# Kernel optimization log

Measured on AMD Instinct MI355X. Metric: run time of the kernel, lower is better.

The kernel has to match this reference:

```python
import jax, jax.numpy as jnp
import numpy as np

N = 50000  # nodes


def gcn_layer(x, src, dst, W, b):
    """DGL GraphConv with norm='both': D_in^{-1/2} A^T D_out^{-1/2} x W + b."""
    E = src.shape[0]
    ones = jnp.ones((E,), dtype=x.dtype)
    deg_out = jax.ops.segment_sum(ones, src, num_segments=N)  # out-degree of src nodes
    deg_in = jax.ops.segment_sum(ones, dst, num_segments=N)   # in-degree of dst nodes
    norm_src = jax.lax.rsqrt(jnp.maximum(deg_out, 1.0))
    norm_dst = jax.lax.rsqrt(jnp.maximum(deg_in, 1.0))
    h = x * norm_src[:, None]
    agg = jax.ops.segment_sum(h[src], dst, num_segments=N)  # [N, in_dim]
    return (agg @ W) * norm_dst[:, None] + b


def encoder(feat, src, dst, W1, b1, W2, b2):
    h = jax.nn.relu(gcn_layer(feat, src, dst, W1, b1))
    h = jax.nn.relu(gcn_layer(h, src, dst, W2, b2))
    return h


def proj(h, fc1_W, fc1_b, fc2_W, fc2_b):
    z = jax.nn.elu(h @ fc1_W + fc1_b)
    return z @ fc2_W + fc2_b


def setup_inputs() -> dict:
    key = jax.random.key(0)
    ks = jax.random.split(key, 12)
    in_dim, hid, out_dim, E = 128, 128, 128, 800000
    inp = {
        "feat1": jax.random.normal(ks[0], (N, in_dim), dtype=jnp.float32),
        "feat2": jax.random.normal(ks[1], (N, in_dim), dtype=jnp.float32),
        "edge_index1": jax.random.randint(ks[2], (2, E), 0, N),
        "edge_index2": jax.random.randint(ks[3], (2, E), 0, N),
        # GraphConv weights: in_dim -> 2*hid -> hid
        "conv1_W": jax.random.normal(ks[4], (in_dim, 2 * hid), dtype=jnp.float32) * 0.05,
        "conv1_b": jnp.zeros((2 * hid,), dtype=jnp.float32),
        "conv2_W": jax.random.normal(ks[5], (2 * hid, hid), dtype=jnp.float32) * 0.05,
        "conv2_b": jnp.zeros((hid,), dtype=jnp.float32),
        # MLP proj: fc1 hid->out, fc2 out->hid
        "fc1_W": jax.random.normal(ks[6], (hid, out_dim), dtype=jnp.float32) * 0.05,
        "fc1_b": jnp.zeros((out_dim,), dtype=jnp.float32),
        "fc2_W": jax.random.normal(ks[7], (out_dim, hid), dtype=jnp.float32) * 0.05,
        "fc2_b": jnp.zeros((hid,), dtype=jnp.float32),
    }
    return inp


def reference(feat1, feat2, edge_index1, edge_index2,
              conv1_W, conv1_b, conv2_W, conv2_b,
              fc1_W, fc1_b, fc2_W, fc2_b):
    h1 = encoder(feat1, edge_index1[0], edge_index1[1], conv1_W, conv1_b, conv2_W, conv2_b)
    h2 = encoder(feat2, edge_index2[0], edge_index2[1], conv1_W, conv1_b, conv2_W, conv2_b)
    z1 = proj(h1, fc1_W, fc1_b, fc2_W, fc2_b)
    z2 = proj(h2, fc1_W, fc1_b, fc2_W, fc2_b)
    return (z1, z2)
```

## Files before the change

### kernel.cpp

```cpp
#include <hip/hip_runtime.h>
#include <math.h>

#define NDIM 128
#define H2   256
#define MAXG 2
#define TPE  8192
#define NBKMAX 512

typedef __attribute__((ext_vector_type(8))) short bf16x8;
typedef __attribute__((ext_vector_type(4))) float f32x4;

__device__ __forceinline__ unsigned short f2bf(float f) {
    unsigned int u = __float_as_uint(f);
    u += 0x7fffu + ((u >> 16) & 1u);
    return (unsigned short)(u >> 16);
}
__device__ __forceinline__ float bf2f(unsigned short h) {
    return __uint_as_float(((unsigned int)h) << 16);
}
__device__ __forceinline__ void split2(float f, unsigned short& h, unsigned short& l) {
    h = f2bf(f);
    l = f2bf(f - bf2f(h));
}

struct BinArgs {
    const int* src[MAXG]; const int* dst[MAXG];
    int* histD[MAXG]; int* histS[MAXG];
    int* totD[MAXG];  int* baseD[MAXG];
    int* totS[MAXG];  int* baseS[MAXG];
    unsigned int* pairs[MAXG];
    unsigned short* srcS[MAXG];
    int E[MAXG]; int NBK; int NT; int n;
};

__global__ __launch_bounds__(256) void binA(BinArgs a) {
    __shared__ int cntD[NBKMAX], cntS[NBKMAX];
    int g = blockIdx.y, t = blockIdx.x, tid = threadIdx.x;
    for (int b = tid; b < NBKMAX; b += 256) { cntD[b] = 0; cntS[b] = 0; }
    __syncthreads();
    int E = a.E[g];
    int base = t * TPE;
#pragma unroll
    for (int k = 0; k < TPE / 256; ++k) {
        int e = base + k * 256 + tid;
        if (e < E) {
            atomicAdd(&cntD[a.dst[g][e] >> 7], 1);
            atomicAdd(&cntS[a.src[g][e] >> 7], 1);
        }
    }
    __syncthreads();
    for (int b = tid; b < a.NBK; b += 256) {
        a.histD[g][t * a.NBK + b] = cntD[b];
        a.histS[g][t * a.NBK + b] = cntS[b];
    }
}

__global__ __launch_bounds__(512) void binB(BinArgs a) {
    int g = blockIdx.y, side = blockIdx.z;
    int* hist = side ? a.histS[g] : a.histD[g];
    int* tot  = side ? a.totS[g]  : a.totD[g];
    int* base = side ? a.baseS[g] : a.baseD[g];
    __shared__ int s[512];
    int b = threadIdx.x;
    int v = 0;
    if (b < a.NBK)
        for (int t = 0; t < a.NT; ++t) v += hist[t * a.NBK + b];
    s[b] = v;
    __syncthreads();
    for (int off = 1; off < 512; off <<= 1) {
        int u = (b >= off) ? s[b - off] : 0;
        __syncthreads();
        s[b] += u;
        __syncthreads();
    }
    int excl = s[b] - v;
    if (b < a.NBK) {
        tot[b] = v;
        base[b] = excl;
        int run = excl;
        for (int t = 0; t < a.NT; ++t) {
            int h = hist[t * a.NBK + b];
            hist[t * a.NBK + b] = run;
            run += h;
        }
    }
}

__global__ __launch_bounds__(256) void binC(BinArgs a) {
    __shared__ int offD[NBKMAX], offS[NBKMAX];
    int g = blockIdx.y, t = blockIdx.x, tid = threadIdx.x;
    for (int b = tid; b < a.NBK; b += 256) {
        offD[b] = a.histD[g][t * a.NBK + b];
        offS[b] = a.histS[g][t * a.NBK + b];
    }
    __syncthreads();
    int E = a.E[g];
    int base = t * TPE;
    unsigned int* pairs = a.pairs[g];
    unsigned short* ss = a.srcS[g];
#pragma unroll
    for (int k = 0; k < TPE / 256; ++k) {
        int e = base + k * 256 + tid;
        if (e < E) {
            int s = a.src[g][e], d = a.dst[g][e];
            int pos = atomicAdd(&offD[d >> 7], 1);
            pairs[pos] = ((unsigned int)(d & 127) << 16) | (unsigned int)s;
            int posS = atomicAdd(&offS[s >> 7], 1);
            ss[posS] = (unsigned short)s;
        }
    }
}

struct FinArgs {
    const unsigned int* pairs[MAXG];
    const unsigned short* srcS[MAXG];
    const int* totD[MAXG]; const int* baseD[MAXG];
    const int* totS[MAXG]; const int* baseS[MAXG];
    int* row_ptr[MAXG]; int* row_end[MAXG];
    unsigned short* edge_srt[MAXG];
    float* ns[MAXG]; float* nd[MAXG];
    int n;
};

__global__ __launch_bounds__(256) void finalize(FinArgs a) {
    __shared__ int cnt[128], hist[128], scn[128], cur[128];
    int g = blockIdx.y, bkt = blockIdx.x, tid = threadIdx.x;
    if (tid < 128) { cnt[tid] = 0; hist[tid] = 0; }
    __syncthreads();
    {
        int base = a.baseS[g][bkt], tot = a.totS[g][bkt];
        const unsigned short* ss = a.srcS[g];
        for (int i = tid; i < tot; i += 256)
            atomicAdd(&cnt[ss[base + i] & 127], 1);
    }
    int cntE = a.totD[g][bkt], base = a.baseD[g][bkt];
    const unsigned int* pp = a.pairs[g] + base;
    for (int i = tid; i < cntE; i += 256)
        atomicAdd(&hist[pp[i] >> 16], 1);
    __syncthreads();
    if (tid < 128) {
        int node = bkt * 128 + tid;
        if (node < a.n) {
            int c = cnt[tid];
            a.ns[g][node] = rsqrtf((float)(c > 1 ? c : 1));
        }
        scn[tid] = hist[tid];
    }
    __syncthreads();
    for (int off = 1; off < 128; off <<= 1) {
        int v = (tid < 128 && tid >= off) ? scn[tid - off] : 0;
        __syncthreads();
        if (tid < 128) scn[tid] += v;
        __syncthreads();
    }
    if (tid < 128) {
        int incl = scn[tid];
        int h = hist[tid];
        cur[tid] = incl - h;
        int node = bkt * 128 + tid;
        if (node < a.n) {
            a.row_ptr[g][node] = base + incl - h;
            a.row_end[g][node] = base + incl;
            a.nd[g][node] = rsqrtf((float)(h > 1 ? h : 1));
        }
    }
    __syncthreads();
    for (int i = tid; i < cntE; i += 256) {
        unsigned int p = pp[i];
        int pos = atomicAdd(&cur[p >> 16], 1);
        a.edge_srt[g][base + pos] = (unsigned short)(p & 0xFFFF);
    }
}

struct GatherArgs {
    const float* X[MAXG];
    const int* row_ptr[MAXG]; const int* row_end[MAXG];
    const unsigned short* edge_src[MAXG];
    const float* nd[MAXG];
    const float* sns[MAXG];
    unsigned short* outH[MAXG]; unsigned short* outL[MAXG];
    const float* bias; int use_nd; int use_sns; int n;
};

__global__ __launch_bounds__(256) void gather_split_b(GatherArgs a) {
    int g = blockIdx.y;
    int half = threadIdx.x >> 5;
    int lane = threadIdx.x & 31;
    int r = blockIdx.x * 8 + half;
    if (r >= a.n) return;
    int j = a.row_ptr[g][r];
    int end = a.row_end[g][r];
    const unsigned short* ep = a.edge_src[g];
    const float* X = a.X[g];
    const float* sns = a.sns[g];
    int base = lane * 4;
    float4 acc = make_float4(0.f, 0.f, 0.f, 0.f);
    if (a.use_sns) {
        for (; j + 3 < end; j += 4) {
            int s0 = ep[j], s1 = ep[j + 1], s2 = ep[j + 2], s3 = ep[j + 3];
            float n0 = sns[s0], n1 = sns[s1], n2 = sns[s2], n3 = sns[s3];
            float4 v0 = *(const float4*)(X + (size_t)s0 * NDIM + base);
            float4 v1 = *(const float4*)(X + (size_t)s1 * NDIM + base);
            float4 v2 = *(const float4*)(X + (size_t)s2 * NDIM + base);
            float4 v3 = *(const float4*)(X + (size_t)s3 * NDIM + base);
            acc.x = fmaf(v0.x, n0, fmaf(v1.x, n1, fmaf(v2.x, n2, fmaf(v3.x, n3, acc.x))));
            acc.y = fmaf(v0.y, n0, fmaf(v1.y, n1, fmaf(v2.y, n2, fmaf(v3.y, n3, acc.y))));
            acc.z = fmaf(v0.z, n0, fmaf(v1.z, n1, fmaf(v2.z, n2, fmaf(v3.z, n3, acc.z))));
            acc.w = fmaf(v0.w, n0, fmaf(v1.w, n1, fmaf(v2.w, n2, fmaf(v3.w, n3, acc.w))));
        }
        for (; j < end; ++j) {
            int s0 = ep[j];
            float n0 = sns[s0];
            float4 v0 = *(const float4*)(X + (size_t)s0 * NDIM + base);
            acc.x = fmaf(v0.x, n0, acc.x); acc.y = fmaf(v0.y, n0, acc.y);
            acc.z = fmaf(v0.z, n0, acc.z); acc.w = fmaf(v0.w, n0, acc.w);
        }
    } else {
        for (; j + 3 < end; j += 4) {
            int s0 = ep[j], s1 = ep[j + 1], s2 = ep[j + 2], s3 = ep[j + 3];
            float4 v0 = *(const float4*)(X + (size_t)s0 * NDIM + base);
            float4 v1 = *(const float4*)(X + (size_t)s1 * NDIM + base);
            float4 v2 = *(const float4*)(X + (size_t)s2 * NDIM + base);
            float4 v3 = *(const float4*)(X + (size_t)s3 * NDIM + base);
            acc.x += v0.x + v1.x + v2.x + v3.x;
            acc.y += v0.y + v1.y + v2.y + v3.y;
            acc.z += v0.z + v1.z + v2.z + v3.z;
            acc.w += v0.w + v1.w + v2.w + v3.w;
        }
        for (; j < end; ++j) {
            int s0 = ep[j];
            float4 v0 = *(const float4*)(X + (size_t)s0 * NDIM + base);
            acc.x += v0.x; acc.y += v0.y; acc.z += v0.z; acc.w += v0.w;
        }
    }
    float v[4] = {acc.x, acc.y, acc.z, acc.w};
    if (a.use_nd) {
        float s = a.nd[g][r];
#pragma unroll
        for (int i = 0; i < 4; ++i)
            v[i] = fmaxf(v[i] * s + a.bias[base + i], 0.f);
    }
    unsigned short h[4], l[4];
#pragma unroll
    for (int i = 0; i < 4; ++i) split2(v[i], h[i], l[i]);
    *(ushort4*)(a.outH[g] + (size_t)r * NDIM + base) = make_ushort4(h[0], h[1], h[2], h[3]);
    *(ushort4*)(a.outL[g] + (size_t)r * NDIM + base) = make_ushort4(l[0], l[1], l[2], l[3]);
}

__global__ void wprep_all(const float* __restrict__ W1, const float* __restrict__ W2,
                          const float* __restrict__ F1, const float* __restrict__ F2,
                          unsigned short* __restrict__ W1h, unsigned short* __restrict__ W1l,
                          unsigned short* __restrict__ W2h, unsigned short* __restrict__ W2l,
                          unsigned short* __restrict__ F1h, unsigned short* __restrict__ F1l,
                          unsigned short* __restrict__ F2h, unsigned short* __restrict__ F2l) {
    int i = blockIdx.x * 256 + threadIdx.x;
    const float* Wsrc; unsigned short *Hd, *Ld; int K, Nc, idx;
    if (i < 32768)       { Wsrc = W1; Hd = W1h; Ld = W1l; K = 128; Nc = 256; idx = i; }
    else if (i < 65536)  { Wsrc = W2; Hd = W2h; Ld = W2l; K = 256; Nc = 128; idx = i - 32768; }
    else if (i < 81920)  { Wsrc = F1; Hd = F1h; Ld = F1l; K = 128; Nc = 128; idx = i - 65536; }
    else                 { Wsrc = F2; Hd = F2h; Ld = F2l; K = 128; Nc = 128; idx = i - 81920; }
    int k = idx / Nc, n = idx % Nc;
    unsigned short h, l;
    split2(Wsrc[idx], h, l);
    Hd[n * K + k] = h;
    Ld[n * K + k] = l;
}

struct GemmArgs {
    const unsigned short* Ah[MAXG]; const unsigned short* Al[MAXG];
    const unsigned short* Bh; const unsigned short* Bl;
    float* C[MAXG]; unsigned short* CH[MAXG]; unsigned short* CL[MAXG];
    const float* rsOut[MAXG]; const float* bOut;
    int M, K, Nc, act, has_rs, has_b, split_out;
};

template <int KT>
__global__ __launch_bounds__(256) void mfma_gemm_s(GemmArgs a) {
    constexpr int LDA = KT + 8;
    __shared__ __align__(16) unsigned short As_h[64 * LDA];
    __shared__ __align__(16) unsigned short As_l[64 * LDA];

    int g = blockIdx.z;
    const unsigned short* __restrict__ Ah_g = a.Ah[g];
    const unsigned short* __restrict__ Al_g = a.Al[g];
    const unsigned short* __restrict__ Bh = a.Bh;
    const unsigned short* __restrict__ Bl = a.Bl;

    int tid  = threadIdx.x;
    int wave = tid >> 6, lane = tid & 63;
    int quad = lane >> 4, l16 = lane & 15;
    int rowBase = blockIdx.x * 64;
    int colBase = blockIdx.y * 128;
    int M = a.M, Nc = a.Nc;

    f32x4 acc[4][2] = {};

    size_t boff[2];
#pragma unroll
    for (int j = 0; j < 2; ++j)
        boff[j] = (size_t)(colBase + wave * 32 + j * 16 + l16) * KT + quad * 8;

    bf16x8 bh[2][4], bl[2][4];
#pragma unroll
    for (int j = 0; j < 2; ++j)
#pragma unroll
        for (int kt = 0; kt < 4; ++kt) {
            bh[j][kt] = *(const bf16x8*)(Bh + boff[j] + kt * 32);
            bl[j][kt] = *(const bf16x8*)(Bl + boff[j] + kt * 32);
        }

    constexpr int CPR = KT / 8;
#pragma unroll
    for (int c0 = 0; c0 < 64 * CPR; c0 += 256) {
        int c = c0 + tid;
        int row = c / CPR;
        int col = (c - row * CPR) * 8;
        int gr = rowBase + row;
        uint4 vh = make_uint4(0, 0, 0, 0), vl = make_uint4(0, 0, 0, 0);
        if (gr < M) {
            vh = *(const uint4*)(Ah_g + (size_t)gr * KT + col);
            vl = *(const uint4*)(Al_g + (size_t)gr * KT + col);
        }
        *(uint4*)(As_h + row * LDA + col) = vh;
        *(uint4*)(As_l + row * LDA + col) = vl;
    }
    __syncthreads();

#pragma unroll
    for (int p = 0; p < KT / 128; ++p) {
        if (p) {
#pragma unroll
            for (int j = 0; j < 2; ++j)
#pragma unroll
                for (int kt = 0; kt < 4; ++kt) {
                    bh[j][kt] = *(const bf16x8*)(Bh + boff[j] + p * 128 + kt * 32);
                    bl[j][kt] = *(const bf16x8*)(Bl + boff[j] + p * 128 + kt * 32);
                }
        }
#pragma unroll
        for (int kt = 0; kt < 4; ++kt) {
            int kc = p * 128 + kt * 32 + quad * 8;
            bf16x8 af[4], alf[4];
#pragma unroll
            for (int i = 0; i < 4; ++i) {
                af[i]  = *(const bf16x8*)(As_h + (i * 16 + l16) * LDA + kc);
                alf[i] = *(const bf16x8*)(As_l + (i * 16 + l16) * LDA + kc);
            }
#pragma unroll
            for (int i = 0; i < 4; ++i)
#pragma unroll
                for (int j = 0; j < 2; ++j) {
                    acc[i][j] = __builtin_amdgcn_mfma_f32_16x16x32_bf16(af[i],  bh[j][kt], acc[i][j], 0, 0, 0);
                    acc[i][j] = __builtin_amdgcn_mfma_f32_16x16x32_bf16(alf[i], bh[j][kt], acc[i][j], 0, 0, 0);
                    acc[i][j] = __builtin_amdgcn_mfma_f32_16x16x32_bf16(af[i],  bl[j][kt], acc[i][j], 0, 0, 0);
                }
        }
    }

#pragma unroll
    for (int i = 0; i < 4; ++i) {
#pragma unroll
        for (int r = 0; r < 4; ++r) {
            int row = rowBase + i * 16 + quad * 4 + r;
            if (row >= M) continue;
            float rs = a.has_rs ? a.rsOut[g][row] : 1.0f;
#pragma unroll
            for (int j = 0; j < 2; ++j) {
                int col = colBase + wave * 32 + j * 16 + l16;
                float v = acc[i][j][r] * rs;
                if (a.has_b) v += a.bOut[col];
                if (a.act == 1) v = fmaxf(v, 0.f);
                else if (a.act == 2) v = v > 0.f ? v : expm1f(v);
                if (a.split_out) {
                    unsigned short h, l;
                    split2(v, h, l);
                    a.CH[g][(size_t)row * Nc + col] = h;
                    a.CL[g][(size_t)row * Nc + col] = l;
                } else {
                    a.C[g][(size_t)row * Nc + col] = v;
                }
            }
        }
    }
}

extern "C" void kernel_launch(void* const* d_in, const int* in_sizes, int n_in,
                              void* d_out, int out_size, void* d_ws, size_t ws_size,
                              hipStream_t stream) {
    const float* feat[2] = {(const float*)d_in[0], (const float*)d_in[1]};
    const int*   ei[2]   = {(const int*)d_in[2], (const int*)d_in[3]};
    const float* W1   = (const float*)d_in[4];
    const float* b1   = (const float*)d_in[5];
    const float* W2   = (const float*)d_in[6];
    const float* b2   = (const float*)d_in[7];
    const float* fc1W = (const float*)d_in[8];
    const float* fc1b = (const float*)d_in[9];
    const float* fc2W = (const float*)d_in[10];
    const float* fc2b = (const float*)d_in[11];
    int N = in_sizes[0] / NDIM;
    float* out = (float*)d_out;

    int Emax = 0;
    for (int g = 0; g < 2; ++g) { int E = in_sizes[2 + g] / 2; if (E > Emax) Emax = E; }
    int NBK = (N + 127) / 128;
    int NT  = (Emax + TPE - 1) / TPE;

    char* p = (char*)d_ws;
    float* ns_[2]; float* nd_[2];
    for (int i = 0; i < 2; ++i) { ns_[i] = (float*)p; p += (size_t)N * 4; }
    for (int i = 0; i < 2; ++i) { nd_[i] = (float*)p; p += (size_t)N * 4; }
    int* rp_[2]; int* re_[2]; unsigned short* esrt_[2];
    for (int i = 0; i < 2; ++i) { rp_[i] = (int*)p; p += (size_t)N * 4; }
    for (int i = 0; i < 2; ++i) { re_[i] = (int*)p; p += (size_t)N * 4; }
    for (int i = 0; i < 2; ++i) { esrt_[i] = (unsigned short*)p; p += (size_t)Emax * 2; }
    unsigned short* R1[2]; unsigned short* R2[2];
    for (int i = 0; i < 2; ++i) { R1[i] = (unsigned short*)p; p += (size_t)N * NDIM * 2 * 2; }
    for (int i = 0; i < 2; ++i) { R2[i] = (unsigned short*)p; p += (size_t)N * H2 * 2 * 2; }
    unsigned short* W1th = (unsigned short*)p; p += (size_t)NDIM * H2 * 2;
    unsigned short* W1tl = (unsigned short*)p; p += (size_t)NDIM * H2 * 2;
    unsigned short* W2th = (unsigned short*)p; p += (size_t)H2 * NDIM * 2;
    unsigned short* W2tl = (unsigned short*)p; p += (size_t)H2 * NDIM * 2;
    unsigned short* f1th = (unsigned short*)p; p += (size_t)NDIM * NDIM * 2;
    unsigned short* f1tl = (unsigned short*)p; p += (size_t)NDIM * NDIM * 2;
    unsigned short* f2th = (unsigned short*)p; p += (size_t)NDIM * NDIM * 2;
    unsigned short* f2tl = (unsigned short*)p; p += (size_t)NDIM * NDIM * 2;
    int* tb = (int*)p; p += (size_t)2 * 4 * NBK * 4;

    int* histD_[2]; int* histS_[2]; unsigned int* pairs_[2]; unsigned short* srcS_[2];
    for (int i = 0; i < 2; ++i) {
        histD_[i] = (int*)R2[i];
        histS_[i] = (int*)R2[i] + (size_t)NT * NBK;
        pairs_[i] = (unsigned int*)((char*)R2[i] + (1 << 20));
        srcS_[i]  = (unsigned short*)R1[i];
    }

    BinArgs ba = {};
    ba.NBK = NBK; ba.NT = NT; ba.n = N;
    for (int i = 0; i < 2; ++i) {
        int E = in_sizes[2 + i] / 2;
        ba.src[i] = ei[i]; ba.dst[i] = ei[i] + E; ba.E[i] = E;
        ba.histD[i] = histD_[i]; ba.histS[i] = histS_[i];
        ba.totD[i]  = tb + (size_t)i * 4 * NBK;
        ba.baseD[i] = tb + (size_t)i * 4 * NBK + NBK;
        ba.totS[i]  = tb + (size_t)i * 4 * NBK + 2 * NBK;
        ba.baseS[i] = tb + (size_t)i * 4 * NBK + 3 * NBK;
        ba.pairs[i] = pairs_[i]; ba.srcS[i] = srcS_[i];
    }

    wprep_all<<<384, 256, 0, stream>>>(W1, W2, fc1W, fc2W,
                                       W1th, W1tl, W2th, W2tl, f1th, f1tl, f2th, f2tl);
    binA<<<dim3(NT, 2), 256, 0, stream>>>(ba);
    binB<<<dim3(1, 2, 2), 512, 0, stream>>>(ba);
    binC<<<dim3(NT, 2), 256, 0, stream>>>(ba);

    FinArgs fa = {};
    fa.n = N;
    for (int i = 0; i < 2; ++i) {
        fa.pairs[i] = pairs_[i]; fa.srcS[i] = srcS_[i];
        fa.totD[i] = ba.totD[i]; fa.baseD[i] = ba.baseD[i];
        fa.totS[i] = ba.totS[i]; fa.baseS[i] = ba.baseS[i];
        fa.row_ptr[i] = rp_[i]; fa.row_end[i] = re_[i];
        fa.edge_srt[i] = esrt_[i];
        fa.ns[i] = ns_[i]; fa.nd[i] = nd_[i];
    }
    finalize<<<dim3(NBK, 2), 256, 0, stream>>>(fa);

    unsigned short *A1h[2], *A1l[2], *X1h[2], *X1l[2], *Gh[2], *Gl[2], *Zh[2], *Zl[2];
    float* T[2];
    for (int i = 0; i < 2; ++i) {
        A1h[i] = R1[i]; A1l[i] = R1[i] + (size_t)N * NDIM;
        T[i]   = (float*)R1[i];
        Zh[i]  = R1[i]; Zl[i]  = R1[i] + (size_t)N * NDIM;
        X1h[i] = R2[i]; X1l[i] = R2[i] + (size_t)N * H2;
        Gh[i]  = R2[i]; Gl[i]  = R2[i] + (size_t)N * NDIM;
    }

    int ggrid = (N + 7) / 8;
    int mgrid = (N + 63) / 64;

    GatherArgs ga = {};
    ga.n = N; ga.use_nd = 0; ga.use_sns = 1; ga.bias = b2;
    for (int i = 0; i < 2; ++i) {
        ga.X[i] = feat[i];
        ga.row_ptr[i] = rp_[i]; ga.row_end[i] = re_[i]; ga.edge_src[i] = esrt_[i];
        ga.nd[i] = nd_[i]; ga.sns[i] = ns_[i];
        ga.outH[i] = A1h[i]; ga.outL[i] = A1l[i];
    }
    gather_split_b<<<dim3(ggrid, 2), 256, 0, stream>>>(ga);

    GemmArgs g1 = {};
    g1.Bh = W1th; g1.Bl = W1tl; g1.bOut = b1;
    g1.M = N; g1.K = NDIM; g1.Nc = H2; g1.act = 1; g1.has_rs = 1; g1.has_b = 1; g1.split_out = 1;
    for (int i = 0; i < 2; ++i) {
        g1.Ah[i] = A1h[i]; g1.Al[i] = A1l[i];
        g1.CH[i] = X1h[i]; g1.CL[i] = X1l[i]; g1.rsOut[i] = nd_[i];
    }
    mfma_gemm_s<128><<<dim3(mgrid, H2 / 128, 2), 256, 0, stream>>>(g1);

    GemmArgs g2 = {};
    g2.Bh = W2th; g2.Bl = W2tl;
    g2.M = N; g2.K = H2; g2.Nc = NDIM; g2.act = 0; g2.has_rs = 1; g2.has_b = 0; g2.split_out = 0;
    for (int i = 0; i < 2; ++i) {
        g2.Ah[i] = X1h[i]; g2.Al[i] = X1l[i]; g2.C[i] = T[i]; g2.rsOut[i] = ns_[i];
    }
    mfma_gemm_s<256><<<dim3(mgrid, 1, 2), 256, 0, stream>>>(g2);

    GatherArgs gb = ga;
    gb.use_nd = 1; gb.use_sns = 0;
    for (int i = 0; i < 2; ++i) {
        gb.X[i] = T[i];
        gb.outH[i] = Gh[i]; gb.outL[i] = Gl[i];
    }
    gather_split_b<<<dim3(ggrid, 2), 256, 0, stream>>>(gb);

    GemmArgs g3 = {};
    g3.Bh = f1th; g3.Bl = f1tl; g3.bOut = fc1b;
    g3.M = N; g3.K = NDIM; g3.Nc = NDIM; g3.act = 2; g3.has_rs = 0; g3.has_b = 1; g3.split_out = 1;
    for (int i = 0; i < 2; ++i) {
        g3.Ah[i] = Gh[i]; g3.Al[i] = Gl[i];
        g3.CH[i] = Zh[i]; g3.CL[i] = Zl[i];
    }
    mfma_gemm_s<128><<<dim3(mgrid, 1, 2), 256, 0, stream>>>(g3);

    GemmArgs g4 = {};
    g4.Bh = f2th; g4.Bl = f2tl; g4.bOut = fc2b;
    g4.M = N; g4.K = NDIM; g4.Nc = NDIM; g4.act = 0; g4.has_rs = 0; g4.has_b = 1; g4.split_out = 0;
    for (int i = 0; i < 2; ++i) {
        g4.Ah[i] = Zh[i]; g4.Al[i] = Zl[i];
        g4.C[i] = out + (size_t)i * N * NDIM;
    }
    mfma_gemm_s<128><<<dim3(mgrid, 1, 2), 256, 0, stream>>>(g4);
}
```

Baseline: 683.2 us.

## Fuse back-to-back GEMM pairs into one kernel keeping intermediate in LDS

Replaces the four separate split-bf16 MFMA GEMM launches with two fused kernels. Each fused kernel computes the first GEMM, applies scale, bias and activation, splits the result into hi/lo bf16 in shared memory, then runs the second GEMM on that tile. This removes the global-memory write and re-read of the 256-wide and 128-wide intermediates and two launches. In exchange it needs more shared memory and registers per block (256-wide accumulators), which may lower occupancy. B operands are now reloaded from global inside each k-step instead of being preloaded into registers.

Result: faster. 590.5 us (-13.6%).

```diff
diff --git a/kernel.cpp b/kernel.cpp
--- a/kernel.cpp
+++ b/kernel.cpp
@@ -266,119 +266,155 @@
     Ld[n * K + k] = l;
 }
 
-struct GemmArgs {
+struct FusedArgs {
     const unsigned short* Ah[MAXG]; const unsigned short* Al[MAXG];
-    const unsigned short* Bh; const unsigned short* Bl;
-    float* C[MAXG]; unsigned short* CH[MAXG]; unsigned short* CL[MAXG];
-    const float* rsOut[MAXG]; const float* bOut;
-    int M, K, Nc, act, has_rs, has_b, split_out;
+    const unsigned short* B1h; const unsigned short* B1l;
+    const unsigned short* B2h; const unsigned short* B2l;
+    const float* rs1[MAXG];
+    const float* rs2[MAXG];
+    const float* b1v;
+    const float* b2v;
+    float* C[MAXG];
+    int M, has_rs1, has_rs2, has_b1, has_b2;
 };
 
-template <int KT>
-__global__ __launch_bounds__(256) void mfma_gemm_s(GemmArgs a) {
-    constexpr int LDA = KT + 8;
-    __shared__ __align__(16) unsigned short As_h[64 * LDA];
-    __shared__ __align__(16) unsigned short As_l[64 * LDA];
-
-    int g = blockIdx.z;
+template <int K1, int N1, int ACT1>
+__global__ __launch_bounds__(256) void fused_gemm2(FusedArgs a) {
+    constexpr int LDA = K1 + 8;
+    constexpr int LDX = N1 + 8;
+    constexpr int SH_A = 64 * LDA;
+    constexpr int SH_X = 64 * LDX;
+    constexpr int SH = (2 * SH_A > 2 * SH_X) ? 2 * SH_A : 2 * SH_X;
+    __shared__ __align__(16) unsigned short S[SH];
+    unsigned short* As_h = S;
+    unsigned short* As_l = S + SH_A;
+    unsigned short* Xs_h = S;
+    unsigned short* Xs_l = S + SH_X;
+
+    int g = blockIdx.y;
     const unsigned short* __restrict__ Ah_g = a.Ah[g];
     const unsigned short* __restrict__ Al_g = a.Al[g];
-    const unsigned short* __restrict__ Bh = a.Bh;
-    const unsigned short* __restrict__ Bl = a.Bl;
 
     int tid  = threadIdx.x;
     int wave = tid >> 6, lane = tid & 63;
     int quad = lane >> 4, l16 = lane & 15;
     int rowBase = blockIdx.x * 64;
-    int colBase = blockIdx.y * 128;
-    int M = a.M, Nc = a.Nc;
-
-    f32x4 acc[4][2] = {};
-
-    size_t boff[2];
-#pragma unroll
-    for (int j = 0; j < 2; ++j)
-        boff[j] = (size_t)(colBase + wave * 32 + j * 16 + l16) * KT + quad * 8;
-
-    bf16x8 bh[2][4], bl[2][4];
-#pragma unroll
-    for (int j = 0; j < 2; ++j)
-#pragma unroll
-        for (int kt = 0; kt < 4; ++kt) {
-            bh[j][kt] = *(const bf16x8*)(Bh + boff[j] + kt * 32);
-            bl[j][kt] = *(const bf16x8*)(Bl + boff[j] + kt * 32);
-        }
-
-    constexpr int CPR = KT / 8;
+    int M = a.M;
+
+    constexpr int CPR = K1 / 8;
 #pragma unroll
     for (int c0 = 0; c0 < 64 * CPR; c0 += 256) {
         int c = c0 + tid;
         int row = c / CPR;
-        int col = (c - row * CPR) * 8;
+        int col = (c % CPR) * 8;
         int gr = rowBase + row;
         uint4 vh = make_uint4(0, 0, 0, 0), vl = make_uint4(0, 0, 0, 0);
         if (gr < M) {
-            vh = *(const uint4*)(Ah_g + (size_t)gr * KT + col);
-            vl = *(const uint4*)(Al_g + (size_t)gr * KT + col);
+            vh = *(const uint4*)(Ah_g + (size_t)gr * K1 + col);
+            vl = *(const uint4*)(Al_g + (size_t)gr * K1 + col);
         }
         *(uint4*)(As_h + row * LDA + col) = vh;
         *(uint4*)(As_l + row * LDA + col) = vl;
     }
     __syncthreads();
 
-#pragma unroll
-    for (int p = 0; p < KT / 128; ++p) {
-        if (p) {
-#pragma unroll
-            for (int j = 0; j < 2; ++j)
-#pragma unroll
-                for (int kt = 0; kt < 4; ++kt) {
-                    bh[j][kt] = *(const bf16x8*)(Bh + boff[j] + p * 128 + kt * 32);
-                    bl[j][kt] = *(const bf16x8*)(Bl + boff[j] + p * 128 + kt * 32);
-                }
-        }
-#pragma unroll
-        for (int kt = 0; kt < 4; ++kt) {
-            int kc = p * 128 + kt * 32 + quad * 8;
-            bf16x8 af[4], alf[4];
-#pragma unroll
-            for (int i = 0; i < 4; ++i) {
-                af[i]  = *(const bf16x8*)(As_h + (i * 16 + l16) * LDA + kc);
-                alf[i] = *(const bf16x8*)(As_l + (i * 16 + l16) * LDA + kc);
+    constexpr int J1 = N1 / 64;
+    int wcol1 = wave * (N1 / 4);
+    f32x4 acc1[4][J1] = {};
+#pragma unroll
+    for (int kt = 0; kt < K1 / 32; ++kt) {
+        int kc = kt * 32 + quad * 8;
+        bf16x8 af[4], alf[4];
+#pragma unroll
+        for (int i = 0; i < 4; ++i) {
+            af[i]  = *(const bf16x8*)(As_h + (i * 16 + l16) * LDA + kc);
+            alf[i] = *(const bf16x8*)(As_l + (i * 16 + l16) * LDA + kc);
+        }
+        bf16x8 bh_[J1], bl_[J1];
+#pragma unroll
+        for (int j = 0; j < J1; ++j) {
+            size_t bo = (size_t)(wcol1 + j * 16 + l16) * K1 + kt * 32 + quad * 8;
+            bh_[j] = *(const bf16x8*)(a.B1h + bo);
+            bl_[j] = *(const bf16x8*)(a.B1l + bo);
+        }
+#pragma unroll
+        for (int i = 0; i < 4; ++i)
+#pragma unroll
+            for (int j = 0; j < J1; ++j) {
+                acc1[i][j] = __builtin_amdgcn_mfma_f32_16x16x32_bf16(af[i],  bh_[j], acc1[i][j], 0, 0, 0);
+                acc1[i][j] = __builtin_amdgcn_mfma_f32_16x16x32_bf16(alf[i], bh_[j], acc1[i][j], 0, 0, 0);
+                acc1[i][j] = __builtin_amdgcn_mfma_f32_16x16x32_bf16(af[i],  bl_[j], acc1[i][j], 0, 0, 0);
             }
-#pragma unroll
-            for (int i = 0; i < 4; ++i)
-#pragma unroll
-                for (int j = 0; j < 2; ++j) {
-                    acc[i][j] = __builtin_amdgcn_mfma_f32_16x16x32_bf16(af[i],  bh[j][kt], acc[i][j], 0, 0, 0);
-                    acc[i][j] = __builtin_amdgcn_mfma_f32_16x16x32_bf16(alf[i], bh[j][kt], acc[i][j], 0, 0, 0);
-                    acc[i][j] = __builtin_amdgcn_mfma_f32_16x16x32_bf16(af[i],  bl[j][kt], acc[i][j], 0, 0, 0);
-                }
-        }
-    }
-
+    }
+    __syncthreads();
+
+    const float* rs1p = a.has_rs1 ? a.rs1[g] : nullptr;
 #pragma unroll
     for (int i = 0; i < 4; ++i) {
 #pragma unroll
         for (int r = 0; r < 4; ++r) {
-            int row = rowBase + i * 16 + quad * 4 + r;
-            if (row >= M) continue;
-            float rs = a.has_rs ? a.rsOut[g][row] : 1.0f;
+            int row  = i * 16 + quad * 4 + r;
+            int grow = rowBase + row;
+            float rs = 1.0f;
+            if (rs1p) rs = (grow < M) ? rs1p[grow] : 0.0f;
+#pragma unroll
+            for (int j = 0; j < J1; ++j) {
+                int col = wcol1 + j * 16 + l16;
+                float v = acc1[i][j][r] * rs;
+                if (a.has_b1) v += a.b1v[col];
+                if (ACT1 == 1) v = fmaxf(v, 0.f);
+                else           v = v > 0.f ? v : expm1f(v);
+                unsigned short h, l;
+                split2(v, h, l);
+                Xs_h[row * LDX + col] = h;
+                Xs_l[row * LDX + col] = l;
+            }
+        }
+    }
+    __syncthreads();
+
+    int wcol2 = wave * 32;
+    f32x4 acc2[4][2] = {};
+#pragma unroll
+    for (int kt = 0; kt < N1 / 32; ++kt) {
+        int kc = kt * 32 + quad * 8;
+        bf16x8 xf[4], xlf[4];
+#pragma unroll
+        for (int i = 0; i < 4; ++i) {
+            xf[i]  = *(const bf16x8*)(Xs_h + (i * 16 + l16) * LDX + kc);
+            xlf[i] = *(const bf16x8*)(Xs_l + (i * 16 + l16) * LDX + kc);
+        }
+        bf16x8 bh_[2], bl_[2];
+#pragma unroll
+        for (int j = 0; j < 2; ++j) {
+            size_t bo = (size_t)(wcol2 + j * 16 + l16) * N1 + kt * 32 + quad * 8;
+            bh_[j] = *(const bf16x8*)(a.B2h + bo);
+            bl_[j] = *(const bf16x8*)(a.B2l + bo);
+        }
+#pragma unroll
+        for (int i = 0; i < 4; ++i)
 #pragma unroll
             for (int j = 0; j < 2; ++j) {
-                int col = colBase + wave * 32 + j * 16 + l16;
-                float v = acc[i][j][r] * rs;
-                if (a.has_b) v += a.bOut[col];
-                if (a.act == 1) v = fmaxf(v, 0.f);
-                else if (a.act == 2) v = v > 0.f ? v : expm1f(v);
-                if (a.split_out) {
-                    unsigned short h, l;
-                    split2(v, h, l);
-                    a.CH[g][(size_t)row * Nc + col] = h;
-                    a.CL[g][(size_t)row * Nc + col] = l;
-                } else {
-                    a.C[g][(size_t)row * Nc + col] = v;
-                }
+                acc2[i][j] = __builtin_amdgcn_mfma_f32_16x16x32_bf16(xf[i],  bh_[j], acc2[i][j], 0, 0, 0);
+                acc2[i][j] = __builtin_amdgcn_mfma_f32_16x16x32_bf16(xlf[i], bh_[j], acc2[i][j], 0, 0, 0);
+                acc2[i][j] = __builtin_amdgcn_mfma_f32_16x16x32_bf16(xf[i],  bl_[j], acc2[i][j], 0, 0, 0);
+            }
+    }
+
+    const float* rs2p = a.has_rs2 ? a.rs2[g] : nullptr;
+#pragma unroll
+    for (int i = 0; i < 4; ++i) {
+#pragma unroll
+        for (int r = 0; r < 4; ++r) {
+            int grow = rowBase + i * 16 + quad * 4 + r;
+            if (grow >= M) continue;
+            float rs = rs2p ? rs2p[grow] : 1.0f;
+#pragma unroll
+            for (int j = 0; j < 2; ++j) {
+                int col = wcol2 + j * 16 + l16;
+                float v = acc2[i][j][r] * rs;
+                if (a.has_b2) v += a.b2v[col];
+                a.C[g][(size_t)grow * NDIM + col] = v;
             }
         }
     }
@@ -465,14 +501,13 @@
     }
     finalize<<<dim3(NBK, 2), 256, 0, stream>>>(fa);
 
-    unsigned short *A1h[2], *A1l[2], *X1h[2], *X1l[2], *Gh[2], *Gl[2], *Zh[2], *Zl[2];
+    unsigned short *A1h[2], *A1l[2], *Gh[2], *Gl[2];
     float* T[2];
     for (int i = 0; i < 2; ++i) {
         A1h[i] = R1[i]; A1l[i] = R1[i] + (size_t)N * NDIM;
-        T[i]   = (float*)R1[i];
-        Zh[i]  = R1[i]; Zl[i]  = R1[i] + (size_t)N * NDIM;
-        X1h[i] = R2[i]; X1l[i] = R2[i] + (size_t)N * H2;
-        Gh[i]  = R2[i]; Gl[i]  = R2[i] + (size_t)N * NDIM;
+        T[i]   = (float*)R2[i];
+        Gh[i]  = R2[i] + (size_t)N * 256;
+        Gl[i]  = R2[i] + (size_t)N * 256 + (size_t)N * NDIM;
     }
 
     int ggrid = (N + 7) / 8;
@@ -488,22 +523,17 @@
     }
     gather_split_b<<<dim3(ggrid, 2), 256, 0, stream>>>(ga);
 
-    GemmArgs g1 = {};
-    g1.Bh = W1th; g1.Bl = W1tl; g1.bOut = b1;
-    g1.M = N; g1.K = NDIM; g1.Nc = H2; g1.act = 1; g1.has_rs = 1; g1.has_b = 1; g1.split_out = 1;
-    for (int i = 0; i < 2; ++i) {
-        g1.Ah[i] = A1h[i]; g1.Al[i] = A1l[i];
-        g1.CH[i] = X1h[i]; g1.CL[i] = X1l[i]; g1.rsOut[i] = nd_[i];
-    }
-    mfma_gemm_s<128><<<dim3(mgrid, H2 / 128, 2), 256, 0, stream>>>(g1);
-
-    GemmArgs g2 = {};
-    g2.Bh = W2th; g2.Bl = W2tl;
-    g2.M = N; g2.K = H2; g2.Nc = NDIM; g2.act = 0; g2.has_rs = 1; g2.has_b = 0; g2.split_out = 0;
-    for (int i = 0; i < 2; ++i) {
-        g2.Ah[i] = X1h[i]; g2.Al[i] = X1l[i]; g2.C[i] = T[i]; g2.rsOut[i] = ns_[i];
-    }
-    mfma_gemm_s<256><<<dim3(mgrid, 1, 2), 256, 0, stream>>>(g2);
+    FusedArgs f12 = {};
+    f12.B1h = W1th; f12.B1l = W1tl; f12.B2h = W2th; f12.B2l = W2tl;
+    f12.b1v = b1; f12.has_b1 = 1; f12.has_b2 = 0;
+    f12.has_rs1 = 1; f12.has_rs2 = 1;
+    f12.M = N;
+    for (int i = 0; i < 2; ++i) {
+        f12.Ah[i] = A1h[i]; f12.Al[i] = A1l[i];
+        f12.rs1[i] = nd_[i]; f12.rs2[i] = ns_[i];
+        f12.C[i] = T[i];
+    }
+    fused_gemm2<128, 256, 1><<<dim3(mgrid, 2), 256, 0, stream>>>(f12);
 
     GatherArgs gb = ga;
     gb.use_nd = 1; gb.use_sns = 0;
@@ -513,21 +543,14 @@
     }
     gather_split_b<<<dim3(ggrid, 2), 256, 0, stream>>>(gb);
 
-    GemmArgs g3 = {};
-    g3.Bh = f1th; g3.Bl = f1tl; g3.bOut = fc1b;
-    g3.M = N; g3.K = NDIM; g3.Nc = NDIM; g3.act = 2; g3.has_rs = 0; g3.has_b = 1; g3.split_out = 1;
-    for (int i = 0; i < 2; ++i) {
-        g3.Ah[i] = Gh[i]; g3.Al[i] = Gl[i];
-        g3.CH[i] = Zh[i]; g3.CL[i] = Zl[i];
-    }
-    mfma_gemm_s<128><<<dim3(mgrid, 1, 2), 256, 0, stream>>>(g3);
-
-    GemmArgs g4 = {};
-    g4.Bh = f2th; g4.Bl = f2tl; g4.bOut = fc2b;
-    g4.M = N; g4.K = NDIM; g4.Nc = NDIM; g4.act = 0; g4.has_rs = 0; g4.has_b = 1; g4.split_out = 0;
-    for (int i = 0; i < 2; ++i) {
-        g4.Ah[i] = Zh[i]; g4.Al[i] = Zl[i];
-        g4.C[i] = out + (size_t)i * N * NDIM;
-    }
-    mfma_gemm_s<128><<<dim3(mgrid, 1, 2), 256, 0, stream>>>(g4);
-}
+    FusedArgs f34 = {};
+    f34.B1h = f1th; f34.B1l = f1tl; f34.B2h = f2th; f34.B2l = f2tl;
+    f34.b1v = fc1b; f34.has_b1 = 1; f34.b2v = fc2b; f34.has_b2 = 1;
+    f34.has_rs1 = 0; f34.has_rs2 = 0;
+    f34.M = N;
+    for (int i = 0; i < 2; ++i) {
+        f34.Ah[i] = Gh[i]; f34.Al[i] = Gl[i];
+        f34.C[i] = out + (size_t)i * N * NDIM;
+    }
+    fused_gemm2<128, 128, 2><<<dim3(mgrid, 2), 256, 0, stream>>>(f34);
+}
```
